# Kernel optimization log

Hardware: AMD Instinct MI355X
Metric: run time of the kernel (lower is better)

Reference implementation:

```python
import jax, jax.numpy as jnp
import numpy as np
from jax.scipy.ndimage import map_coordinates

N_ANGLES = 120


def _radon3d(vol):
    """Faithful port of radon_transform_3d_pet(axis=2 path) + radon_torch_2d.

    vol: [1, 1, D, H, W].  Slices are vol[:, :, :, d] (dim 3), stacked over
    range(W) -- valid because H == W here.  Returns sinogram stack [S, A, L].
    """
    B, C, D, H, W = vol.shape  # B = C = 1
    imgs = jnp.moveaxis(vol[0, 0], 1, 0)  # [S=H, D, W]; slice s = vol[0,0,:,s,:]

    L = int(np.ceil(np.sqrt(D * D + W * W)))  # padded square canvas
    top = (L - D) // 2   # pad_h // 2
    left = (L - W) // 2  # pad_w // 2

    angles = jnp.linspace(0.0, 120.0, N_ANGLES) * (jnp.pi / 180.0)
    cos_t, sin_t = jnp.cos(angles), jnp.sin(angles)

    # affine_grid with align_corners=True over an L x L output
    lin = jnp.linspace(-1.0, 1.0, L)
    xg, yg = jnp.meshgrid(lin, lin)  # [L, L]; xg varies along columns
    x_in = cos_t[:, None, None] * xg - sin_t[:, None, None] * yg  # [A, L, L]
    y_in = sin_t[:, None, None] * xg + cos_t[:, None, None] * yg
    # unnormalize (align_corners=True) and shift into the UNpadded image frame;
    # zeros in the pad region == map_coordinates mode='constant', cval=0
    ix = (x_in + 1.0) * 0.5 * (L - 1) - left  # column coord into [D, W] image
    iy = (y_in + 1.0) * 0.5 * (L - 1) - top   # row coord

    def sample(im):  # im: [D, W] -> rotated canvases [A, L, L]
        return map_coordinates(im, [iy, ix], order=1, mode='constant', cval=0.0)

    rot = jax.vmap(sample)(imgs)        # [S, A, L, L]
    return rot.sum(axis=2)              # sum over rows -> [S, A, L]


def setup_inputs() -> dict:
    key = jax.random.key(0)
    k1, k2 = jax.random.split(key)
    shape = (1, 1, 64, 64, 64)
    out = jax.random.uniform(k1, shape, dtype=jnp.float32)
    gt = jax.random.uniform(k2, shape, dtype=jnp.float32)
    return {"out": out, "gt": gt}


def reference(out, gt):
    so = _radon3d(out)  # [S, A, L]
    sg = _radon3d(gt)
    # sum over slices of per-slice mean L1 (matches the Python loop of F.l1_loss)
    return jnp.abs(so - sg).mean(axis=(1, 2)).sum()
```

## Files before the change

### kernel.cpp

```cpp
#include <hip/hip_runtime.h>
#include <hip/hip_fp16.h>

#define DD 64
#define NA 120
#define NS 64
#define LL 91
#define PS 67
#define PSTR 69
#define NCELL (PS * PSTR)
#define NSL 4
#define NANG 4
#define JT 96
#define NTHR (NANG * JT)
#define NBLKS ((NS / NSL) * (NA / NANG))

static __device__ __forceinline__ __half2 u2h(unsigned int u) {
    union { unsigned int u; __half2 h; } v; v.u = u; return v.h;
}
static __device__ __forceinline__ unsigned int h2u(__half2 h) {
    union { __half2 h; unsigned int u; } v; v.h = h; return v.u;
}

__global__ __launch_bounds__(NTHR, 4) void radon_loss_kernel(
    const float* __restrict__ vout, const float* __restrict__ vgt,
    float* __restrict__ out)
{
    __shared__ unsigned int P0[NCELL];
    __shared__ unsigned int P1[NCELL];
    __shared__ float wsum[NTHR / 64];

    const int bid = blockIdx.x;
    const int sp = bid / (NA / NANG);
    const int ap = bid - sp * (NA / NANG);
    const int s0 = sp * NSL;
    const int t = threadIdx.x;

    for (int idx = t; idx < NCELL; idx += NTHR) {
        P0[idx] = 0u;
        P1[idx] = 0u;
    }
    __syncthreads();

    for (int idx = t; idx < DD * DD; idx += NTHR) {
        const int d = idx >> 6, w = idx & 63;
        const int g = d * 4096 + s0 * 64 + w;
        const float d0 = vout[g]       - vgt[g];
        const float d1 = vout[g + 64]  - vgt[g + 64];
        const float d2 = vout[g + 128] - vgt[g + 128];
        const float d3 = vout[g + 192] - vgt[g + 192];
        const int ci = (d + 1) * PSTR + (w + 1);
        P0[ci] = h2u(__floats2half2_rn(d0, d1));
        P1[ci] = h2u(__floats2half2_rn(d2, d3));
    }
    __syncthreads();

    const int ja = t / JT;
    const int j  = t - ja * JT;
    const int a  = ap * NANG + ja;
    const float theta = (float)a * (float)(3.14159265358979323846 * 120.0 / 119.0 / 180.0);
    const float c = cosf(theta), sn = sinf(theta);

    float val = 0.f;
    if (j < LL) {
        const float linj = fmaf((float)j, 2.0f / 90.0f, -1.0f);
        const float bx1 = fmaf(c,  linj, 1.0f) * 45.0f - 12.0f + 45.0f * sn;
        const float by1 = fmaf(sn, linj, 1.0f) * 45.0f - 12.0f - 45.0f * c;
        __half2 acc0 = __floats2half2_rn(0.f, 0.f);
        __half2 acc1 = acc0;
        for (int i = 0; i < LL; ++i) {
            const float xs = fminf(fmaxf(fmaf(-(float)i, sn, bx1), 0.0f), 65.0f);
            const float ys = fminf(fmaxf(fmaf( (float)i, c,  by1), 0.0f), 65.0f);
            const int ix = (int)xs;
            const int iy = (int)ys;
            const float wx = xs - (float)ix;
            const float wy = ys - (float)iy;
            const __half2 wx2 = __float2half2_rn(wx);
            const __half2 wy2 = __float2half2_rn(wy);
            const int ci = iy * PSTR + ix;
            const unsigned int a00 = P0[ci],        a01 = P0[ci + 1];
            const unsigned int a10 = P0[ci + PSTR], a11 = P0[ci + PSTR + 1];
            const unsigned int b00 = P1[ci],        b01 = P1[ci + 1];
            const unsigned int b10 = P1[ci + PSTR], b11 = P1[ci + PSTR + 1];
            const __half2 t0 = __hfma2(wx2, __hsub2(u2h(a01), u2h(a00)), u2h(a00));
            const __half2 bb0 = __hfma2(wx2, __hsub2(u2h(a11), u2h(a10)), u2h(a10));
            acc0 = __hadd2(acc0, __hfma2(wy2, __hsub2(bb0, t0), t0));
            const __half2 t1 = __hfma2(wx2, __hsub2(u2h(b01), u2h(b00)), u2h(b00));
            const __half2 bb1 = __hfma2(wx2, __hsub2(u2h(b11), u2h(b10)), u2h(b10));
            acc1 = __hadd2(acc1, __hfma2(wy2, __hsub2(bb1, t1), t1));
        }
        const float2 a0f = __half22float2(acc0);
        const float2 a1f = __half22float2(acc1);
        val = fabsf(a0f.x) + fabsf(a0f.y) + fabsf(a1f.x) + fabsf(a1f.y);
    }

    #pragma unroll
    for (int off = 32; off > 0; off >>= 1)
        val += __shfl_down(val, off);
    const int wave = t >> 6, lane = t & 63;
    if (lane == 0) wsum[wave] = val;
    __syncthreads();
    if (t == 0) {
        float v = 0.f;
        #pragma unroll
        for (int wv = 0; wv < NTHR / 64; ++wv) v += wsum[wv];
        atomicAdd(out, v * (1.0f / (float)(NA * LL)));
    }
}

extern "C" void kernel_launch(void* const* d_in, const int* in_sizes, int n_in,
                              void* d_out, int out_size, void* d_ws, size_t ws_size,
                              hipStream_t stream) {
    const float* vout = (const float*)d_in[0];
    const float* vgt  = (const float*)d_in[1];
    float* out = (float*)d_out;

    hipMemsetAsync(out, 0, sizeof(float), stream);
    radon_loss_kernel<<<NBLKS, NTHR, 0, stream>>>(vout, vgt, out);
}
```

Measured before the change: 85.18 us.

## Split ray integration into two halves across blocks with a separate finalize kernel

The per-ray row loop is split at row 46 into two halves, each run by its own set of blocks, which doubles the grid to 960 blocks. Partial sums go to a workspace buffer, and a second kernel combines the halves, takes absolute values and reduces with atomics. The launch-bounds occupancy hint rises from 4 to 6. The intent is more parallelism and better latency hiding on the long serial loop. The cost is staging the volume into shared memory twice, an extra kernel launch, and a global round trip for the partials.

Result: slower. 89.38 us (+4.9%).

```diff
diff --git a/kernel.cpp b/kernel.cpp
--- a/kernel.cpp
+++ b/kernel.cpp
@@ -12,7 +12,12 @@
 #define NANG 4
 #define JT 96
 #define NTHR (NANG * JT)
-#define NBLKS ((NS / NSL) * (NA / NANG))
+#define NSP (NS / NSL)
+#define NAP (NA / NANG)
+#define NBLK_HALF (NSP * NAP)
+#define NBLKS (2 * NBLK_HALF)
+#define IH_SPLIT 46
+#define PHALF (NSP * NA * JT)
 
 static __device__ __forceinline__ __half2 u2h(unsigned int u) {
     union { unsigned int u; __half2 h; } v; v.u = u; return v.h;
@@ -21,19 +26,20 @@
     union { __half2 h; unsigned int u; } v; v.h = h; return v.u;
 }
 
-__global__ __launch_bounds__(NTHR, 4) void radon_loss_kernel(
+__global__ __launch_bounds__(NTHR, 6) void radon_half_kernel(
     const float* __restrict__ vout, const float* __restrict__ vgt,
-    float* __restrict__ out)
+    float4* __restrict__ part)
 {
     __shared__ unsigned int P0[NCELL];
     __shared__ unsigned int P1[NCELL];
-    __shared__ float wsum[NTHR / 64];
 
     const int bid = blockIdx.x;
-    const int sp = bid / (NA / NANG);
-    const int ap = bid - sp * (NA / NANG);
-    const int s0 = sp * NSL;
-    const int t = threadIdx.x;
+    const int h   = bid / NBLK_HALF;
+    const int rem = bid - h * NBLK_HALF;
+    const int sp  = rem / NAP;
+    const int ap  = rem - sp * NAP;
+    const int s0  = sp * NSL;
+    const int t   = threadIdx.x;
 
     for (int idx = t; idx < NCELL; idx += NTHR) {
         P0[idx] = 0u;
@@ -60,14 +66,15 @@
     const float theta = (float)a * (float)(3.14159265358979323846 * 120.0 / 119.0 / 180.0);
     const float c = cosf(theta), sn = sinf(theta);
 
-    float val = 0.f;
     if (j < LL) {
         const float linj = fmaf((float)j, 2.0f / 90.0f, -1.0f);
         const float bx1 = fmaf(c,  linj, 1.0f) * 45.0f - 12.0f + 45.0f * sn;
         const float by1 = fmaf(sn, linj, 1.0f) * 45.0f - 12.0f - 45.0f * c;
+        const int i0 = h ? IH_SPLIT : 0;
+        const int i1 = h ? LL : IH_SPLIT;
         __half2 acc0 = __floats2half2_rn(0.f, 0.f);
         __half2 acc1 = acc0;
-        for (int i = 0; i < LL; ++i) {
+        for (int i = i0; i < i1; ++i) {
             const float xs = fminf(fmaxf(fmaf(-(float)i, sn, bx1), 0.0f), 65.0f);
             const float ys = fminf(fmaxf(fmaf( (float)i, c,  by1), 0.0f), 65.0f);
             const int ix = (int)xs;
@@ -81,29 +88,45 @@
             const unsigned int a10 = P0[ci + PSTR], a11 = P0[ci + PSTR + 1];
             const unsigned int b00 = P1[ci],        b01 = P1[ci + 1];
             const unsigned int b10 = P1[ci + PSTR], b11 = P1[ci + PSTR + 1];
-            const __half2 t0 = __hfma2(wx2, __hsub2(u2h(a01), u2h(a00)), u2h(a00));
+            const __half2 t0  = __hfma2(wx2, __hsub2(u2h(a01), u2h(a00)), u2h(a00));
             const __half2 bb0 = __hfma2(wx2, __hsub2(u2h(a11), u2h(a10)), u2h(a10));
             acc0 = __hadd2(acc0, __hfma2(wy2, __hsub2(bb0, t0), t0));
-            const __half2 t1 = __hfma2(wx2, __hsub2(u2h(b01), u2h(b00)), u2h(b00));
+            const __half2 t1  = __hfma2(wx2, __hsub2(u2h(b01), u2h(b00)), u2h(b00));
             const __half2 bb1 = __hfma2(wx2, __hsub2(u2h(b11), u2h(b10)), u2h(b10));
             acc1 = __hadd2(acc1, __hfma2(wy2, __hsub2(bb1, t1), t1));
         }
         const float2 a0f = __half22float2(acc0);
         const float2 a1f = __half22float2(acc1);
-        val = fabsf(a0f.x) + fabsf(a0f.y) + fabsf(a1f.x) + fabsf(a1f.y);
+        part[h * PHALF + (sp * NA + a) * JT + j] =
+            make_float4(a0f.x, a0f.y, a1f.x, a1f.y);
     }
+}
 
+#define NENT (NSP * NA * LL)
+
+__global__ __launch_bounds__(256) void finalize_kernel(
+    const float4* __restrict__ part, float* __restrict__ out)
+{
+    __shared__ float wsum[4];
+    float v = 0.f;
+    for (int e = blockIdx.x * 256 + threadIdx.x; e < NENT; e += gridDim.x * 256) {
+        const int spa = e / LL;
+        const int j   = e - spa * LL;
+        const int pi  = spa * JT + j;
+        const float4 p0 = part[pi];
+        const float4 p1 = part[PHALF + pi];
+        v += fabsf(p0.x + p1.x) + fabsf(p0.y + p1.y)
+           + fabsf(p0.z + p1.z) + fabsf(p0.w + p1.w);
+    }
     #pragma unroll
     for (int off = 32; off > 0; off >>= 1)
-        val += __shfl_down(val, off);
-    const int wave = t >> 6, lane = t & 63;
-    if (lane == 0) wsum[wave] = val;
+        v += __shfl_down(v, off);
+    const int wave = threadIdx.x >> 6, lane = threadIdx.x & 63;
+    if (lane == 0) wsum[wave] = v;
     __syncthreads();
-    if (t == 0) {
-        float v = 0.f;
-        #pragma unroll
-        for (int wv = 0; wv < NTHR / 64; ++wv) v += wsum[wv];
-        atomicAdd(out, v * (1.0f / (float)(NA * LL)));
+    if (threadIdx.x == 0) {
+        const float s = wsum[0] + wsum[1] + wsum[2] + wsum[3];
+        atomicAdd(out, s * (1.0f / (float)(NA * LL)));
     }
 }
 
@@ -113,7 +136,9 @@
     const float* vout = (const float*)d_in[0];
     const float* vgt  = (const float*)d_in[1];
     float* out = (float*)d_out;
+    float4* part = (float4*)d_ws;
 
     hipMemsetAsync(out, 0, sizeof(float), stream);
-    radon_loss_kernel<<<NBLKS, NTHR, 0, stream>>>(vout, vgt, out);
+    radon_half_kernel<<<NBLKS, NTHR, 0, stream>>>(vout, vgt, part);
+    finalize_kernel<<<240, 256, 0, stream>>>(part, out);
 }
```

## Pack neighbor columns into uint4 LDS cells and double angles per block

Applied to the files above, without the earlier changes.

Shared memory now stores each cell as a uint4 holding its own four-slice half2 pair plus the right neighbor's, so each bilinear sample needs two 128-bit LDS reads instead of eight 32-bit reads. Angles per block rise from 4 to 8, halving the block count so each staged slab serves more threads, and the launch-bounds occupancy hint is dropped. The trade-off is double the LDS footprint (~74KB per block), which limits resident blocks per CU, and a 128-bit stride that may cause bank conflicts.

Result: faster. 77.79 us (-8.7%).

```diff
diff --git a/kernel.cpp b/kernel.cpp
--- a/kernel.cpp
+++ b/kernel.cpp
@@ -9,10 +9,12 @@
 #define PSTR 69
 #define NCELL (PS * PSTR)
 #define NSL 4
-#define NANG 4
+#define NANG 8
 #define JT 96
 #define NTHR (NANG * JT)
-#define NBLKS ((NS / NSL) * (NA / NANG))
+#define NSP (NS / NSL)
+#define NAP (NA / NANG)
+#define NBLKS (NSP * NAP)
 
 static __device__ __forceinline__ __half2 u2h(unsigned int u) {
     union { unsigned int u; __half2 h; } v; v.u = u; return v.h;
@@ -21,24 +23,21 @@
     union { __half2 h; unsigned int u; } v; v.h = h; return v.u;
 }
 
-__global__ __launch_bounds__(NTHR, 4) void radon_loss_kernel(
+__global__ __launch_bounds__(NTHR) void radon_loss_kernel(
     const float* __restrict__ vout, const float* __restrict__ vgt,
     float* __restrict__ out)
 {
-    __shared__ unsigned int P0[NCELL];
-    __shared__ unsigned int P1[NCELL];
+    __shared__ uint4 C[NCELL];
     __shared__ float wsum[NTHR / 64];
 
     const int bid = blockIdx.x;
-    const int sp = bid / (NA / NANG);
-    const int ap = bid - sp * (NA / NANG);
+    const int sp = bid / NAP;
+    const int ap = bid - sp * NAP;
     const int s0 = sp * NSL;
     const int t = threadIdx.x;
 
-    for (int idx = t; idx < NCELL; idx += NTHR) {
-        P0[idx] = 0u;
-        P1[idx] = 0u;
-    }
+    for (int idx = t; idx < NCELL; idx += NTHR)
+        C[idx] = make_uint4(0u, 0u, 0u, 0u);
     __syncthreads();
 
     for (int idx = t; idx < DD * DD; idx += NTHR) {
@@ -48,9 +47,12 @@
         const float d1 = vout[g + 64]  - vgt[g + 64];
         const float d2 = vout[g + 128] - vgt[g + 128];
         const float d3 = vout[g + 192] - vgt[g + 192];
-        const int ci = (d + 1) * PSTR + (w + 1);
-        P0[ci] = h2u(__floats2half2_rn(d0, d1));
-        P1[ci] = h2u(__floats2half2_rn(d2, d3));
+        uint2 v8;
+        v8.x = h2u(__floats2half2_rn(d0, d1));
+        v8.y = h2u(__floats2half2_rn(d2, d3));
+        const int rb = (d + 1) * PSTR + w;
+        ((uint2*)&C[rb + 1])[0] = v8;
+        ((uint2*)&C[rb])[1]     = v8;
     }
     __syncthreads();
 
@@ -65,8 +67,8 @@
         const float linj = fmaf((float)j, 2.0f / 90.0f, -1.0f);
         const float bx1 = fmaf(c,  linj, 1.0f) * 45.0f - 12.0f + 45.0f * sn;
         const float by1 = fmaf(sn, linj, 1.0f) * 45.0f - 12.0f - 45.0f * c;
-        __half2 acc0 = __floats2half2_rn(0.f, 0.f);
-        __half2 acc1 = acc0;
+        __half2 acc01 = __floats2half2_rn(0.f, 0.f);
+        __half2 acc23 = acc01;
         for (int i = 0; i < LL; ++i) {
             const float xs = fminf(fmaxf(fmaf(-(float)i, sn, bx1), 0.0f), 65.0f);
             const float ys = fminf(fmaxf(fmaf( (float)i, c,  by1), 0.0f), 65.0f);
@@ -77,20 +79,18 @@
             const __half2 wx2 = __float2half2_rn(wx);
             const __half2 wy2 = __float2half2_rn(wy);
             const int ci = iy * PSTR + ix;
-            const unsigned int a00 = P0[ci],        a01 = P0[ci + 1];
-            const unsigned int a10 = P0[ci + PSTR], a11 = P0[ci + PSTR + 1];
-            const unsigned int b00 = P1[ci],        b01 = P1[ci + 1];
-            const unsigned int b10 = P1[ci + PSTR], b11 = P1[ci + PSTR + 1];
-            const __half2 t0 = __hfma2(wx2, __hsub2(u2h(a01), u2h(a00)), u2h(a00));
-            const __half2 bb0 = __hfma2(wx2, __hsub2(u2h(a11), u2h(a10)), u2h(a10));
-            acc0 = __hadd2(acc0, __hfma2(wy2, __hsub2(bb0, t0), t0));
-            const __half2 t1 = __hfma2(wx2, __hsub2(u2h(b01), u2h(b00)), u2h(b00));
-            const __half2 bb1 = __hfma2(wx2, __hsub2(u2h(b11), u2h(b10)), u2h(b10));
-            acc1 = __hadd2(acc1, __hfma2(wy2, __hsub2(bb1, t1), t1));
+            const uint4 q0 = C[ci];
+            const uint4 q1 = C[ci + PSTR];
+            const __half2 t01 = __hfma2(wx2, __hsub2(u2h(q0.z), u2h(q0.x)), u2h(q0.x));
+            const __half2 b01 = __hfma2(wx2, __hsub2(u2h(q1.z), u2h(q1.x)), u2h(q1.x));
+            acc01 = __hadd2(acc01, __hfma2(wy2, __hsub2(b01, t01), t01));
+            const __half2 t23 = __hfma2(wx2, __hsub2(u2h(q0.w), u2h(q0.y)), u2h(q0.y));
+            const __half2 b23 = __hfma2(wx2, __hsub2(u2h(q1.w), u2h(q1.y)), u2h(q1.y));
+            acc23 = __hadd2(acc23, __hfma2(wy2, __hsub2(b23, t23), t23));
         }
-        const float2 a0f = __half22float2(acc0);
-        const float2 a1f = __half22float2(acc1);
-        val = fabsf(a0f.x) + fabsf(a0f.y) + fabsf(a1f.x) + fabsf(a1f.y);
+        const float2 a01 = __half22float2(acc01);
+        const float2 a23 = __half22float2(acc23);
+        val = fabsf(a01.x) + fabsf(a01.y) + fabsf(a23.x) + fabsf(a23.y);
     }
 
     #pragma unroll
```
